# Performance work log

Measured on AMD Instinct MI355X. Metric: run time of the kernel, lower is better.

The kernel has to match this reference:

```python
import jax, jax.numpy as jnp
import numpy as np

N = 50000   # nodes
E = 1600000 # edges
D = 64      # feature dim


def gcn_conv(x, edge_index, W, b):
    """PyG GCNConv: x' = D^-1/2 (A+I) D^-1/2 (x W) + b."""
    n = x.shape[0]
    xw = x @ W                                   # [N, D_out] linear first (PyG order)
    loop = jnp.arange(n)
    src = jnp.concatenate([edge_index[0], loop])  # add self-loops
    dst = jnp.concatenate([edge_index[1], loop])
    deg = jax.ops.segment_sum(jnp.ones_like(src, dtype=xw.dtype), dst, num_segments=n)
    dinv = jnp.where(deg > 0, jax.lax.rsqrt(deg), 0.0)
    norm = dinv[src] * dinv[dst]                  # symmetric normalization
    out = jax.ops.segment_sum(norm[:, None] * xw[src], dst, num_segments=n)
    return out + b


def setup_inputs() -> dict:
    key = jax.random.key(0)
    k1, k2, k3, k4 = jax.random.split(key, 4)
    x = jax.random.normal(k1, (N, D), dtype=jnp.float32)
    edge_index = jax.random.randint(k2, (2, E), 0, N, dtype=jnp.int64)
    s = 1.0 / np.sqrt(D)
    W1 = jax.random.normal(k3, (D, D), dtype=jnp.float32) * s
    b1 = jnp.zeros((D,), dtype=jnp.float32)
    W2 = jax.random.normal(k4, (D, D), dtype=jnp.float32) * s
    b2 = jnp.zeros((D,), dtype=jnp.float32)
    return {"x": x, "edge_index": edge_index, "W1": W1, "b1": b1, "W2": W2, "b2": b2}


def reference(x, edge_index, W1, b1, W2, b2):
    h = gcn_conv(x, edge_index, W1, b1)
    h = jax.nn.relu(h)  # dropout is identity in eval mode
    out = gcn_conv(h, edge_index, W2, b2)
    return out
```

## Files before the change

kernel.cpp:

```cpp
#include <hip/hip_runtime.h>
#include <hip/hip_fp16.h>


#define P1_EDGES 4096
#define BSTRIDE 16384

typedef float vfloat4 __attribute__((ext_vector_type(4)));

__global__ void bucket_kernel(const int* __restrict__ src, const int* __restrict__ dst,
                              unsigned* __restrict__ cursor, unsigned* __restrict__ ebuf,
                              int e, int B) {
    __shared__ unsigned hist[256];
    __shared__ unsigned base[256];
    for (int i = threadIdx.x; i < B; i += 1024) hist[i] = 0;
    __syncthreads();
    int e0 = blockIdx.x * P1_EDGES;
    int tbase = e0 + (int)threadIdx.x * 4;
    int4 sv = make_int4(0, 0, 0, 0), dv = make_int4(0, 0, 0, 0);
    if (tbase + 3 < e) {
        sv = ((const int4*)(src + e0))[threadIdx.x];
        dv = ((const int4*)(dst + e0))[threadIdx.x];
    } else {
        if (tbase + 0 < e) { sv.x = src[tbase + 0]; dv.x = dst[tbase + 0]; }
        if (tbase + 1 < e) { sv.y = src[tbase + 1]; dv.y = dst[tbase + 1]; }
        if (tbase + 2 < e) { sv.z = src[tbase + 2]; dv.z = dst[tbase + 2]; }
    }
    unsigned bk[4], rk[4], pk[4];
    bool vk[4];
#pragma unroll
    for (int k = 0; k < 4; ++k) {
        int t = tbase + k;
        vk[k] = (t < e);
        bk[k] = 0; rk[k] = 0; pk[k] = 0;
        if (vk[k]) {
            unsigned s = (unsigned)(k == 0 ? sv.x : k == 1 ? sv.y : k == 2 ? sv.z : sv.w);
            unsigned d = (unsigned)(k == 0 ? dv.x : k == 1 ? dv.y : k == 2 ? dv.z : dv.w);
            unsigned b = d >> 8;
            bk[k] = b;
            rk[k] = atomicAdd(&hist[b], 1u);
            pk[k] = (d << 16) | s;
        }
    }
    __syncthreads();
    for (int i = threadIdx.x; i < B; i += 1024)
        base[i] = hist[i] ? atomicAdd(&cursor[i], hist[i]) : 0u;
    __syncthreads();
#pragma unroll
    for (int k = 0; k < 4; ++k)
        if (vk[k]) {
            unsigned slot = base[bk[k]] + rk[k];
            if (slot < (unsigned)BSTRIDE)
                ebuf[(size_t)bk[k] * BSTRIDE + slot] = pk[k];
        }
}

__global__ void statsfill_kernel(const unsigned* __restrict__ ebuf,
                                 const unsigned* __restrict__ bcnt,
                                 unsigned* __restrict__ rpf, float* __restrict__ dinv,
                                 unsigned short* __restrict__ csr, int n, int e) {
    __shared__ unsigned pos[256];
    __shared__ unsigned sh[256];
    __shared__ unsigned rpl[256];
    __shared__ unsigned bs;
    int b = blockIdx.x;
    int w0 = b << 8;
    int wlen = min(w0 + 256, n) - w0;
    unsigned c0 = 0;
    if (threadIdx.x < 256) { c0 = bcnt[threadIdx.x]; sh[threadIdx.x] = c0; }
    __syncthreads();
    for (int off = 1; off < 256; off <<= 1) {
        unsigned t = 0;
        if (threadIdx.x < 256 && threadIdx.x >= (unsigned)off) t = sh[threadIdx.x - off];
        __syncthreads();
        if (threadIdx.x < 256) sh[threadIdx.x] += t;
        __syncthreads();
    }
    if (threadIdx.x == (unsigned)b) bs = sh[b] - c0;
    if (threadIdx.x < 256) pos[threadIdx.x] = 0;
    __syncthreads();
    unsigned cnt = bcnt[b];
    const unsigned* eb = ebuf + (size_t)b * BSTRIDE;
    for (unsigned j = threadIdx.x; j < cnt; j += 1024)
        atomicAdd(&pos[(eb[j] >> 16) - w0], 1u);
    __syncthreads();
    unsigned v = 0;
    if (threadIdx.x < 256) { v = pos[threadIdx.x]; sh[threadIdx.x] = v; }
    __syncthreads();
    for (int off = 1; off < 256; off <<= 1) {
        unsigned t = 0;
        if (threadIdx.x < 256 && threadIdx.x >= (unsigned)off) t = sh[threadIdx.x - off];
        __syncthreads();
        if (threadIdx.x < 256) sh[threadIdx.x] += t;
        __syncthreads();
    }
    if (threadIdx.x < 256) {
        unsigned rp = bs + sh[threadIdx.x] - v;
        rpl[threadIdx.x] = rp;
        if ((int)threadIdx.x < wlen) {
            rpf[w0 + threadIdx.x] = rp;
            dinv[w0 + threadIdx.x] = rsqrtf((float)v + 1.0f);
        }
        pos[threadIdx.x] = 0;
    }
    if (b == (int)gridDim.x - 1 && threadIdx.x == 0) rpf[n] = (unsigned)e;
    __syncthreads();
    for (unsigned j = threadIdx.x; j < cnt; j += 1024) {
        unsigned p = eb[j];
        unsigned d = (p >> 16) - w0;
        unsigned r = atomicAdd(&pos[d], 1u);
        csr[rpl[d] + r] = (unsigned short)(p & 0xffffu);
    }
}

__global__ void gemm64_kernel(const float4* __restrict__ X4, const float* __restrict__ W,
                              const float* __restrict__ dinv, __half* __restrict__ Yh, int n) {
    __shared__ float4 Ws[64][16];
    for (int i = threadIdx.x; i < 64 * 16; i += blockDim.x)
        Ws[i >> 4][i & 15] = ((const float4*)W)[i];
    __syncthreads();
    int lane = threadIdx.x & 63;
    int l = lane & 15;
    int gbase = lane & 48;
    int wid = blockIdx.x * (blockDim.x >> 6) + (threadIdx.x >> 6);
    int row = wid * 4 + (lane >> 4);
    if (row >= n) return;
    float4 xv = X4[(size_t)row * 16 + l];
    float4 acc = make_float4(0.f, 0.f, 0.f, 0.f);
#pragma unroll
    for (int k = 0; k < 64; ++k) {
        float comp = (k & 3) == 0 ? xv.x : (k & 3) == 1 ? xv.y : (k & 3) == 2 ? xv.z : xv.w;
        float a = __shfl(comp, gbase + (k >> 2));
        float4 w = Ws[k][l];
        acc.x = fmaf(a, w.x, acc.x); acc.y = fmaf(a, w.y, acc.y);
        acc.z = fmaf(a, w.z, acc.z); acc.w = fmaf(a, w.w, acc.w);
    }
    float di = dinv[row];
    __half2 h0 = __floats2half2_rn(acc.x * di, acc.y * di);
    __half2 h1 = __floats2half2_rn(acc.z * di, acc.w * di);
    uint2 o;
    o.x = *(const unsigned*)&h0;
    o.y = *(const unsigned*)&h1;
    *(uint2*)(Yh + (size_t)row * 64 + 4 * l) = o;
}

struct f8 { float4 a, b; };

__device__ __forceinline__ f8 aggregate_row8(const __half* __restrict__ xwh,
                                             const unsigned* __restrict__ csrw,
                                             unsigned start, unsigned end,
                                             int row, int l8, int gbase) {
    f8 acc;
    {
        uint4 hv = *(const uint4*)(xwh + (size_t)row * 64 + 8 * l8);
        float2 f0 = __half22float2(*(const __half2*)&hv.x);
        float2 f1 = __half22float2(*(const __half2*)&hv.y);
        float2 f2 = __half22float2(*(const __half2*)&hv.z);
        float2 f3 = __half22float2(*(const __half2*)&hv.w);
        acc.a = make_float4(f0.x, f0.y, f1.x, f1.y);
        acc.b = make_float4(f2.x, f2.y, f3.x, f3.y);
    }
    unsigned wb = start >> 1;
    unsigned jw = wb + (unsigned)l8;
    unsigned ed = (jw * 2 < end) ? __builtin_nontemporal_load(&csrw[jw]) : 0u;
    for (unsigned base = wb; base * 2 < end; base += 8) {
        unsigned jn = base + 8 + (unsigned)l8;
        unsigned ed_next = (jn * 2 < end) ? __builtin_nontemporal_load(&csrw[jn]) : 0u;
#pragma unroll
        for (int t = 0; t < 8; ++t) {
            unsigned p = __shfl(ed, gbase + t);
            unsigned i0 = (base + (unsigned)t) * 2;
            int s0 = (int)(p & 0xffffu);
            int s1 = (int)(p >> 16);
            float w0 = (i0 >= start && i0 < end) ? 1.0f : 0.0f;
            float w1 = (i0 + 1 < end) ? 1.0f : 0.0f;
            uint4 hv0 = *(const uint4*)(xwh + (size_t)s0 * 64 + 8 * l8);
            uint4 hv1 = *(const uint4*)(xwh + (size_t)s1 * 64 + 8 * l8);
            float2 a0 = __half22float2(*(const __half2*)&hv0.x);
            float2 a1 = __half22float2(*(const __half2*)&hv0.y);
            float2 a2 = __half22float2(*(const __half2*)&hv0.z);
            float2 a3 = __half22float2(*(const __half2*)&hv0.w);
            acc.a.x = fmaf(w0, a0.x, acc.a.x); acc.a.y = fmaf(w0, a0.y, acc.a.y);
            acc.a.z = fmaf(w0, a1.x, acc.a.z); acc.a.w = fmaf(w0, a1.y, acc.a.w);
            acc.b.x = fmaf(w0, a2.x, acc.b.x); acc.b.y = fmaf(w0, a2.y, acc.b.y);
            acc.b.z = fmaf(w0, a3.x, acc.b.z); acc.b.w = fmaf(w0, a3.y, acc.b.w);
            float2 c0 = __half22float2(*(const __half2*)&hv1.x);
            float2 c1 = __half22float2(*(const __half2*)&hv1.y);
            float2 c2 = __half22float2(*(const __half2*)&hv1.z);
            float2 c3 = __half22float2(*(const __half2*)&hv1.w);
            acc.a.x = fmaf(w1, c0.x, acc.a.x); acc.a.y = fmaf(w1, c0.y, acc.a.y);
            acc.a.z = fmaf(w1, c1.x, acc.a.z); acc.a.w = fmaf(w1, c1.y, acc.a.w);
            acc.b.x = fmaf(w1, c2.x, acc.b.x); acc.b.y = fmaf(w1, c2.y, acc.b.y);
            acc.b.z = fmaf(w1, c3.x, acc.b.z); acc.b.w = fmaf(w1, c3.y, acc.b.w);
        }
        ed = ed_next;
    }
    return acc;
}

__global__ void gather_gemm_kernel(const __half* __restrict__ xwh, const unsigned* __restrict__ csrw,
                                   const unsigned* __restrict__ row_ptr, const float* __restrict__ dinv,
                                   const float* __restrict__ b1, const float* __restrict__ W2,
                                   __half* __restrict__ Yh, int n) {
    __shared__ float4 Ws[64][16];
    for (int i = threadIdx.x; i < 64 * 16; i += blockDim.x)
        Ws[i >> 4][i & 15] = ((const float4*)W2)[i];
    __syncthreads();
    int lane = threadIdx.x & 63;
    int l8 = lane & 7;
    int gbase = lane & 56;
    int wid = blockIdx.x * (blockDim.x >> 6) + (threadIdx.x >> 6);
    int row = wid * 8 + (lane >> 3);
    if (row >= n) return;
    float di = dinv[row];
    f8 acc = aggregate_row8(xwh, csrw, row_ptr[row], row_ptr[row + 1], row, l8, gbase);
    float4 ba = ((const float4*)b1)[2 * l8];
    float4 bb = ((const float4*)b1)[2 * l8 + 1];
    float h0 = fmaxf(fmaf(di, acc.a.x, ba.x), 0.f);
    float h1 = fmaxf(fmaf(di, acc.a.y, ba.y), 0.f);
    float h2 = fmaxf(fmaf(di, acc.a.z, ba.z), 0.f);
    float h3 = fmaxf(fmaf(di, acc.a.w, ba.w), 0.f);
    float h4 = fmaxf(fmaf(di, acc.b.x, bb.x), 0.f);
    float h5 = fmaxf(fmaf(di, acc.b.y, bb.y), 0.f);
    float h6 = fmaxf(fmaf(di, acc.b.z, bb.z), 0.f);
    float h7 = fmaxf(fmaf(di, acc.b.w, bb.w), 0.f);
    float4 o0 = make_float4(0.f, 0.f, 0.f, 0.f);
    float4 o1 = make_float4(0.f, 0.f, 0.f, 0.f);
#pragma unroll
    for (int k = 0; k < 64; ++k) {
        float comp = (k & 7) == 0 ? h0 : (k & 7) == 1 ? h1 : (k & 7) == 2 ? h2 :
                     (k & 7) == 3 ? h3 : (k & 7) == 4 ? h4 : (k & 7) == 5 ? h5 :
                     (k & 7) == 6 ? h6 : h7;
        float a = __shfl(comp, gbase + (k >> 3));
        float4 w0 = Ws[k][2 * l8];
        float4 w1 = Ws[k][2 * l8 + 1];
        o0.x = fmaf(a, w0.x, o0.x); o0.y = fmaf(a, w0.y, o0.y);
        o0.z = fmaf(a, w0.z, o0.z); o0.w = fmaf(a, w0.w, o0.w);
        o1.x = fmaf(a, w1.x, o1.x); o1.y = fmaf(a, w1.y, o1.y);
        o1.z = fmaf(a, w1.z, o1.z); o1.w = fmaf(a, w1.w, o1.w);
    }
    __half2 p0 = __floats2half2_rn(o0.x * di, o0.y * di);
    __half2 p1 = __floats2half2_rn(o0.z * di, o0.w * di);
    __half2 p2 = __floats2half2_rn(o1.x * di, o1.y * di);
    __half2 p3 = __floats2half2_rn(o1.z * di, o1.w * di);
    uint4 o;
    o.x = *(const unsigned*)&p0; o.y = *(const unsigned*)&p1;
    o.z = *(const unsigned*)&p2; o.w = *(const unsigned*)&p3;
    *(uint4*)(Yh + (size_t)row * 64 + 8 * l8) = o;
}

__global__ void gather_out_kernel(const __half* __restrict__ xwh, const unsigned* __restrict__ csrw,
                                  const unsigned* __restrict__ row_ptr, const float* __restrict__ dinv,
                                  const float* __restrict__ bias, float4* __restrict__ out4, int n) {
    int lane = threadIdx.x & 63;
    int l8 = lane & 7;
    int gbase = lane & 56;
    int wid = blockIdx.x * (blockDim.x >> 6) + (threadIdx.x >> 6);
    int row = wid * 8 + (lane >> 3);
    if (row >= n) return;
    float di = dinv[row];
    f8 acc = aggregate_row8(xwh, csrw, row_ptr[row], row_ptr[row + 1], row, l8, gbase);
    float4 ba = ((const float4*)bias)[2 * l8];
    float4 bb = ((const float4*)bias)[2 * l8 + 1];
    vfloat4 oa, ob;
    oa.x = fmaf(di, acc.a.x, ba.x); oa.y = fmaf(di, acc.a.y, ba.y);
    oa.z = fmaf(di, acc.a.z, ba.z); oa.w = fmaf(di, acc.a.w, ba.w);
    ob.x = fmaf(di, acc.b.x, bb.x); ob.y = fmaf(di, acc.b.y, bb.y);
    ob.z = fmaf(di, acc.b.z, bb.z); ob.w = fmaf(di, acc.b.w, bb.w);
    vfloat4* o4 = (vfloat4*)out4;
    __builtin_nontemporal_store(oa, &o4[(size_t)row * 16 + 2 * l8]);
    __builtin_nontemporal_store(ob, &o4[(size_t)row * 16 + 2 * l8 + 1]);
}

extern "C" void kernel_launch(void* const* d_in, const int* in_sizes, int n_in,
                              void* d_out, int out_size, void* d_ws, size_t ws_size,
                              hipStream_t stream) {
    const float* x  = (const float*)d_in[0];
    const int*   ei = (const int*)d_in[1];
    const float* W1 = (const float*)d_in[2];
    const float* b1 = (const float*)d_in[3];
    const float* W2 = (const float*)d_in[4];
    const float* b2 = (const float*)d_in[5];
    const int n = in_sizes[0] / 64;
    const int e = in_sizes[1] / 2;
    const int* src = ei;
    const int* dst = ei + e;

    char* ws = (char*)d_ws;
    size_t off = 0;
    auto alloc = [&](size_t bytes) -> void* {
        void* p = ws + off;
        off = (off + bytes + 255) & ~(size_t)255;
        return p;
    };
    unsigned* rpf    = (unsigned*)alloc((size_t)(n + 1) * 4);
    float*    dinv   = (float*)alloc((size_t)n * 4);
    unsigned* cursor = (unsigned*)alloc(256 * 4);
    unsigned short* csr = (unsigned short*)alloc(((size_t)e / 2 + 64) * 4);
    const int B = (n + 255) / 256;
    size_t ebuf_sz = (size_t)B * BSTRIDE * 4;
    size_t ov = ebuf_sz > (size_t)n * 64 * 2 ? ebuf_sz : (size_t)n * 64 * 2;
    char*     overlay = (char*)alloc(ov);
    unsigned* ebuf    = (unsigned*)overlay;
    __half*   xwh1    = (__half*)overlay;
    __half*   xwh2    = (__half*)alloc((size_t)n * 64 * 2);
    float*    outf    = (float*)d_out;

    const int nbP1 = (e + P1_EDGES - 1) / P1_EDGES;

    hipMemsetAsync(cursor, 0, 256 * 4, stream);
    bucket_kernel<<<nbP1, 1024, 0, stream>>>(src, dst, cursor, ebuf, e, B);
    statsfill_kernel<<<B, 1024, 0, stream>>>(ebuf, cursor, rpf, dinv, csr, n, e);

    const int gblk16 = (n + 15) / 16;
    const int gblk32 = (n + 31) / 32;

    gemm64_kernel<<<gblk16, 256, 0, stream>>>((const float4*)x, W1, dinv, xwh1, n);
    gather_gemm_kernel<<<gblk32, 256, 0, stream>>>(xwh1, (const unsigned*)csr, rpf, dinv, b1, W2, xwh2, n);

    gather_out_kernel<<<gblk32, 256, 0, stream>>>(xwh2, (const unsigned*)csr, rpf, dinv, b2, (float4*)outf, n);
}
```

Baseline: 174.8 us.

## Replace bucketed CSR build with global-atomic count, scan, and fill

Swaps the two-pass bucket sort (LDS histogram into per-bucket buffers, then per-bucket local scan and fill) for a three-kernel CSR build: global atomic degree count, a block scan to get row pointers, and a fill that uses per-node global atomic cursors. The gather kernels also recompute dinv from row_ptr differences instead of loading it. This drops the large ebuf staging buffer and its write and re-read. In exchange it needs about 3.2M global atomics spread over 50k random addresses, scatters 16-bit writes randomly into csr, and adds a memset and an extra launch.

New measurement: 324.3 us. 85.5% more time.

```diff
diff --git a/kernel.cpp b/kernel.cpp
--- a/kernel.cpp
+++ b/kernel.cpp
@@ -2,113 +2,83 @@
 #include <hip/hip_fp16.h>
 
 
-#define P1_EDGES 4096
-#define BSTRIDE 16384
-
 typedef float vfloat4 __attribute__((ext_vector_type(4)));
 
-__global__ void bucket_kernel(const int* __restrict__ src, const int* __restrict__ dst,
-                              unsigned* __restrict__ cursor, unsigned* __restrict__ ebuf,
-                              int e, int B) {
-    __shared__ unsigned hist[256];
-    __shared__ unsigned base[256];
-    for (int i = threadIdx.x; i < B; i += 1024) hist[i] = 0;
-    __syncthreads();
-    int e0 = blockIdx.x * P1_EDGES;
-    int tbase = e0 + (int)threadIdx.x * 4;
-    int4 sv = make_int4(0, 0, 0, 0), dv = make_int4(0, 0, 0, 0);
-    if (tbase + 3 < e) {
-        sv = ((const int4*)(src + e0))[threadIdx.x];
-        dv = ((const int4*)(dst + e0))[threadIdx.x];
+__global__ void count_kernel(const int* __restrict__ dst, unsigned* __restrict__ deg, int e) {
+    int t4 = blockIdx.x * blockDim.x + threadIdx.x;
+    int base = t4 * 4;
+    if (base + 3 < e) {
+        int4 d = ((const int4*)dst)[t4];
+        atomicAdd(&deg[d.x], 1u); atomicAdd(&deg[d.y], 1u);
+        atomicAdd(&deg[d.z], 1u); atomicAdd(&deg[d.w], 1u);
     } else {
-        if (tbase + 0 < e) { sv.x = src[tbase + 0]; dv.x = dst[tbase + 0]; }
-        if (tbase + 1 < e) { sv.y = src[tbase + 1]; dv.y = dst[tbase + 1]; }
-        if (tbase + 2 < e) { sv.z = src[tbase + 2]; dv.z = dst[tbase + 2]; }
-    }
-    unsigned bk[4], rk[4], pk[4];
-    bool vk[4];
-#pragma unroll
-    for (int k = 0; k < 4; ++k) {
-        int t = tbase + k;
-        vk[k] = (t < e);
-        bk[k] = 0; rk[k] = 0; pk[k] = 0;
-        if (vk[k]) {
-            unsigned s = (unsigned)(k == 0 ? sv.x : k == 1 ? sv.y : k == 2 ? sv.z : sv.w);
-            unsigned d = (unsigned)(k == 0 ? dv.x : k == 1 ? dv.y : k == 2 ? dv.z : dv.w);
-            unsigned b = d >> 8;
-            bk[k] = b;
-            rk[k] = atomicAdd(&hist[b], 1u);
-            pk[k] = (d << 16) | s;
+        for (int i = base; i < e; ++i) atomicAdd(&deg[dst[i]], 1u);
+    }
+}
+
+__global__ void scan_kernel(const unsigned* __restrict__ deg, unsigned* __restrict__ rpf,
+                            float* __restrict__ dinv, unsigned* __restrict__ cursor,
+                            int n, int e, int B) {
+    __shared__ unsigned ws[256];
+    __shared__ unsigned sh[256];
+    __shared__ unsigned bsh;
+    int b = blockIdx.x, tid = threadIdx.x;
+    int w0 = b << 8;
+    unsigned s = 0;
+    if (tid < B) {
+        int wb = tid << 8;
+        int len = min(wb + 256, n) - wb;
+        const uint4* d4 = (const uint4*)(deg + wb);
+        int i = 0;
+        for (; i + 4 <= len; i += 4) { uint4 v = d4[i >> 2]; s += v.x + v.y + v.z + v.w; }
+        for (; i < len; ++i) s += deg[wb + i];
+    }
+    ws[tid] = s;
+    __syncthreads();
+    for (int off = 1; off < 256; off <<= 1) {
+        unsigned t = (tid >= off) ? ws[tid - off] : 0u;
+        __syncthreads();
+        ws[tid] += t;
+        __syncthreads();
+    }
+    if (tid == b) bsh = ws[tid] - s;
+    int wlen = min(w0 + 256, n) - w0;
+    unsigned dv = (tid < wlen) ? deg[w0 + tid] : 0u;
+    sh[tid] = dv;
+    __syncthreads();
+    for (int off = 1; off < 256; off <<= 1) {
+        unsigned t = (tid >= off) ? sh[tid - off] : 0u;
+        __syncthreads();
+        sh[tid] += t;
+        __syncthreads();
+    }
+    if (tid < wlen) {
+        unsigned rp = bsh + sh[tid] - dv;
+        rpf[w0 + tid] = rp;
+        cursor[w0 + tid] = rp;
+        dinv[w0 + tid] = rsqrtf((float)dv + 1.0f);
+    }
+    if (b == (int)gridDim.x - 1 && tid == 0) rpf[n] = (unsigned)e;
+}
+
+__global__ void fill_kernel(const int* __restrict__ src, const int* __restrict__ dst,
+                            unsigned* __restrict__ cursor, unsigned short* __restrict__ csr,
+                            int e) {
+    int t4 = blockIdx.x * blockDim.x + threadIdx.x;
+    int base = t4 * 4;
+    if (base + 3 < e) {
+        int4 s = ((const int4*)src)[t4];
+        int4 d = ((const int4*)dst)[t4];
+        unsigned p;
+        p = atomicAdd(&cursor[d.x], 1u); csr[p] = (unsigned short)s.x;
+        p = atomicAdd(&cursor[d.y], 1u); csr[p] = (unsigned short)s.y;
+        p = atomicAdd(&cursor[d.z], 1u); csr[p] = (unsigned short)s.z;
+        p = atomicAdd(&cursor[d.w], 1u); csr[p] = (unsigned short)s.w;
+    } else {
+        for (int i = base; i < e; ++i) {
+            unsigned p = atomicAdd(&cursor[dst[i]], 1u);
+            csr[p] = (unsigned short)src[i];
         }
-    }
-    __syncthreads();
-    for (int i = threadIdx.x; i < B; i += 1024)
-        base[i] = hist[i] ? atomicAdd(&cursor[i], hist[i]) : 0u;
-    __syncthreads();
-#pragma unroll
-    for (int k = 0; k < 4; ++k)
-        if (vk[k]) {
-            unsigned slot = base[bk[k]] + rk[k];
-            if (slot < (unsigned)BSTRIDE)
-                ebuf[(size_t)bk[k] * BSTRIDE + slot] = pk[k];
-        }
-}
-
-__global__ void statsfill_kernel(const unsigned* __restrict__ ebuf,
-                                 const unsigned* __restrict__ bcnt,
-                                 unsigned* __restrict__ rpf, float* __restrict__ dinv,
-                                 unsigned short* __restrict__ csr, int n, int e) {
-    __shared__ unsigned pos[256];
-    __shared__ unsigned sh[256];
-    __shared__ unsigned rpl[256];
-    __shared__ unsigned bs;
-    int b = blockIdx.x;
-    int w0 = b << 8;
-    int wlen = min(w0 + 256, n) - w0;
-    unsigned c0 = 0;
-    if (threadIdx.x < 256) { c0 = bcnt[threadIdx.x]; sh[threadIdx.x] = c0; }
-    __syncthreads();
-    for (int off = 1; off < 256; off <<= 1) {
-        unsigned t = 0;
-        if (threadIdx.x < 256 && threadIdx.x >= (unsigned)off) t = sh[threadIdx.x - off];
-        __syncthreads();
-        if (threadIdx.x < 256) sh[threadIdx.x] += t;
-        __syncthreads();
-    }
-    if (threadIdx.x == (unsigned)b) bs = sh[b] - c0;
-    if (threadIdx.x < 256) pos[threadIdx.x] = 0;
-    __syncthreads();
-    unsigned cnt = bcnt[b];
-    const unsigned* eb = ebuf + (size_t)b * BSTRIDE;
-    for (unsigned j = threadIdx.x; j < cnt; j += 1024)
-        atomicAdd(&pos[(eb[j] >> 16) - w0], 1u);
-    __syncthreads();
-    unsigned v = 0;
-    if (threadIdx.x < 256) { v = pos[threadIdx.x]; sh[threadIdx.x] = v; }
-    __syncthreads();
-    for (int off = 1; off < 256; off <<= 1) {
-        unsigned t = 0;
-        if (threadIdx.x < 256 && threadIdx.x >= (unsigned)off) t = sh[threadIdx.x - off];
-        __syncthreads();
-        if (threadIdx.x < 256) sh[threadIdx.x] += t;
-        __syncthreads();
-    }
-    if (threadIdx.x < 256) {
-        unsigned rp = bs + sh[threadIdx.x] - v;
-        rpl[threadIdx.x] = rp;
-        if ((int)threadIdx.x < wlen) {
-            rpf[w0 + threadIdx.x] = rp;
-            dinv[w0 + threadIdx.x] = rsqrtf((float)v + 1.0f);
-        }
-        pos[threadIdx.x] = 0;
-    }
-    if (b == (int)gridDim.x - 1 && threadIdx.x == 0) rpf[n] = (unsigned)e;
-    __syncthreads();
-    for (unsigned j = threadIdx.x; j < cnt; j += 1024) {
-        unsigned p = eb[j];
-        unsigned d = (p >> 16) - w0;
-        unsigned r = atomicAdd(&pos[d], 1u);
-        csr[rpl[d] + r] = (unsigned short)(p & 0xffffu);
     }
 }
 
@@ -198,7 +168,7 @@
 }
 
 __global__ void gather_gemm_kernel(const __half* __restrict__ xwh, const unsigned* __restrict__ csrw,
-                                   const unsigned* __restrict__ row_ptr, const float* __restrict__ dinv,
+                                   const unsigned* __restrict__ row_ptr,
                                    const float* __restrict__ b1, const float* __restrict__ W2,
                                    __half* __restrict__ Yh, int n) {
     __shared__ float4 Ws[64][16];
@@ -211,8 +181,9 @@
     int wid = blockIdx.x * (blockDim.x >> 6) + (threadIdx.x >> 6);
     int row = wid * 8 + (lane >> 3);
     if (row >= n) return;
-    float di = dinv[row];
-    f8 acc = aggregate_row8(xwh, csrw, row_ptr[row], row_ptr[row + 1], row, l8, gbase);
+    unsigned start = row_ptr[row], end = row_ptr[row + 1];
+    float di = rsqrtf((float)(end - start) + 1.0f);
+    f8 acc = aggregate_row8(xwh, csrw, start, end, row, l8, gbase);
     float4 ba = ((const float4*)b1)[2 * l8];
     float4 bb = ((const float4*)b1)[2 * l8 + 1];
     float h0 = fmaxf(fmaf(di, acc.a.x, ba.x), 0.f);
@@ -249,7 +220,7 @@
 }
 
 __global__ void gather_out_kernel(const __half* __restrict__ xwh, const unsigned* __restrict__ csrw,
-                                  const unsigned* __restrict__ row_ptr, const float* __restrict__ dinv,
+                                  const unsigned* __restrict__ row_ptr,
                                   const float* __restrict__ bias, float4* __restrict__ out4, int n) {
     int lane = threadIdx.x & 63;
     int l8 = lane & 7;
@@ -257,8 +228,9 @@
     int wid = blockIdx.x * (blockDim.x >> 6) + (threadIdx.x >> 6);
     int row = wid * 8 + (lane >> 3);
     if (row >= n) return;
-    float di = dinv[row];
-    f8 acc = aggregate_row8(xwh, csrw, row_ptr[row], row_ptr[row + 1], row, l8, gbase);
+    unsigned start = row_ptr[row], end = row_ptr[row + 1];
+    float di = rsqrtf((float)(end - start) + 1.0f);
+    f8 acc = aggregate_row8(xwh, csrw, start, end, row, l8, gbase);
     float4 ba = ((const float4*)bias)[2 * l8];
     float4 bb = ((const float4*)bias)[2 * l8 + 1];
     vfloat4 oa, ob;
@@ -294,28 +266,26 @@
     };
     unsigned* rpf    = (unsigned*)alloc((size_t)(n + 1) * 4);
     float*    dinv   = (float*)alloc((size_t)n * 4);
-    unsigned* cursor = (unsigned*)alloc(256 * 4);
+    unsigned* deg    = (unsigned*)alloc((size_t)n * 4);
+    unsigned* cursor = (unsigned*)alloc((size_t)n * 4);
     unsigned short* csr = (unsigned short*)alloc(((size_t)e / 2 + 64) * 4);
+    __half*   xwh1   = (__half*)alloc((size_t)n * 64 * 2);
+    __half*   xwh2   = (__half*)alloc((size_t)n * 64 * 2);
+    float*    outf   = (float*)d_out;
+
     const int B = (n + 255) / 256;
-    size_t ebuf_sz = (size_t)B * BSTRIDE * 4;
-    size_t ov = ebuf_sz > (size_t)n * 64 * 2 ? ebuf_sz : (size_t)n * 64 * 2;
-    char*     overlay = (char*)alloc(ov);
-    unsigned* ebuf    = (unsigned*)overlay;
-    __half*   xwh1    = (__half*)overlay;
-    __half*   xwh2    = (__half*)alloc((size_t)n * 64 * 2);
-    float*    outf    = (float*)d_out;
-
-    const int nbP1 = (e + P1_EDGES - 1) / P1_EDGES;
-
-    hipMemsetAsync(cursor, 0, 256 * 4, stream);
-    bucket_kernel<<<nbP1, 1024, 0, stream>>>(src, dst, cursor, ebuf, e, B);
-    statsfill_kernel<<<B, 1024, 0, stream>>>(ebuf, cursor, rpf, dinv, csr, n, e);
+    const int nbE4 = (e / 4 + 1023) / 1024;
+
+    hipMemsetAsync(deg, 0, (size_t)n * 4, stream);
+    count_kernel<<<nbE4, 1024, 0, stream>>>(dst, deg, e);
+    scan_kernel<<<B, 256, 0, stream>>>(deg, rpf, dinv, cursor, n, e, B);
+    fill_kernel<<<nbE4, 1024, 0, stream>>>(src, dst, cursor, csr, e);
 
     const int gblk16 = (n + 15) / 16;
     const int gblk32 = (n + 31) / 32;
 
     gemm64_kernel<<<gblk16, 256, 0, stream>>>((const float4*)x, W1, dinv, xwh1, n);
-    gather_gemm_kernel<<<gblk32, 256, 0, stream>>>(xwh1, (const unsigned*)csr, rpf, dinv, b1, W2, xwh2, n);
-
-    gather_out_kernel<<<gblk32, 256, 0, stream>>>(xwh2, (const unsigned*)csr, rpf, dinv, b2, (float4*)outf, n);
-}
+    gather_gemm_kernel<<<gblk32, 256, 0, stream>>>(xwh1, (const unsigned*)csr, rpf, b1, W2, xwh2, n);
+
+    gather_out_kernel<<<gblk32, 256, 0, stream>>>(xwh2, (const unsigned*)csr, rpf, b2, (float4*)outf, n);
+}
```
